# Kernel tuning notes

Measured on AMD Instinct MI355X. Metric: run time of the kernel, lower is better.

Reference implementation:

```python
import jax, jax.numpy as jnp
import numpy as np

N = 100000   # nodes
E = 1000000  # edges
G = 256      # graphs
IN, HID, OUT = 64, 64, 32


def _gcn_conv(x, W, b, src, dst, n_nodes):
    # PyG GCNConv with add_self_loops=True, symmetric normalization:
    # out = D^{-1/2} (A + I) D^{-1/2} X W + b
    h = x @ W  # [N, F]
    deg = jax.ops.segment_sum(jnp.ones_like(src, dtype=h.dtype), dst, num_segments=n_nodes) + 1.0
    dinv = jax.lax.rsqrt(deg)  # deg >= 1 due to self loops
    norm = dinv[src] * dinv[dst]  # [E]
    agg = jax.ops.segment_sum(h[src] * norm[:, None], dst, num_segments=n_nodes)
    agg = agg + h * (dinv * dinv)[:, None]  # self-loop contribution
    return agg + b


def setup_inputs() -> dict:
    key = jax.random.key(0)
    ks = jax.random.split(key, 12)
    x = jax.random.normal(ks[0], (N, IN), dtype=jnp.float32)
    edge_index = jax.random.randint(ks[1], (2, E), 0, N, dtype=jnp.int64)
    batch = jnp.sort(jax.random.randint(ks[2], (N,), 0, G, dtype=jnp.int64))

    def lin(k, fin, fout):
        s = 1.0 / np.sqrt(fin)
        kw, kb = jax.random.split(k)
        return (jax.random.uniform(kw, (fin, fout), minval=-s, maxval=s, dtype=jnp.float32),
                jax.random.uniform(kb, (fout,), minval=-s, maxval=s, dtype=jnp.float32))

    W1, b1 = lin(ks[3], IN, HID)
    W2, b2 = lin(ks[4], HID, HID)
    Wmu, bmu = lin(ks[5], HID, OUT)
    Wlv, blv = lin(ks[6], HID, OUT)
    Wd1, bd1 = lin(ks[7], OUT, HID)
    Wd2, bd2 = lin(ks[8], HID, IN)
    return {"x": x, "edge_index": edge_index, "batch": batch,
            "W1": W1, "b1": b1, "W2": W2, "b2": b2,
            "Wmu": Wmu, "bmu": bmu, "Wlv": Wlv, "blv": blv,
            "Wd1": Wd1, "bd1": bd1, "Wd2": Wd2, "bd2": bd2}


def reference(x, edge_index, batch, W1, b1, W2, b2, Wmu, bmu, Wlv, blv, Wd1, bd1, Wd2, bd2):
    src, dst = edge_index[0], edge_index[1]
    h = jax.nn.relu(_gcn_conv(x, W1, b1, src, dst, N))
    h = jax.nn.relu(_gcn_conv(h, W2, b2, src, dst, N))
    # global mean pool per graph
    sums = jax.ops.segment_sum(h, batch, num_segments=G)
    counts = jax.ops.segment_sum(jnp.ones((N,), dtype=h.dtype), batch, num_segments=G)
    pooled = sums / jnp.maximum(counts, 1.0)[:, None]  # [G, HID]
    mu = pooled @ Wmu + bmu
    logvar = pooled @ Wlv + blv
    eps = jax.random.normal(jax.random.key(42), mu.shape, dtype=mu.dtype)
    z = mu + eps * jnp.exp(0.5 * logvar)
    recon = jax.nn.relu(z @ Wd1 + bd1) @ Wd2 + bd2  # [G, IN]
    return recon, mu, logvar
```

## Files before the change

### kernel.cpp

```cpp
#include <hip/hip_runtime.h>
#include <hip/hip_bf16.h>

typedef __attribute__((ext_vector_type(8))) short bf16x8;
typedef __attribute__((ext_vector_type(4))) float f32x4;

__device__ inline unsigned short f2bf(float f) {
    unsigned u = __float_as_uint(f);
    unsigned r = u + 0x7fffu + ((u >> 16) & 1u);
    return (unsigned short)(r >> 16);
}
__device__ inline float bf2f(unsigned short s) {
    return __uint_as_float((unsigned)s << 16);
}


__device__ inline unsigned rotl32(unsigned x, unsigned r) {
    return (x << r) | (x >> (32 - r));
}

__device__ inline void threefry2x32_042(unsigned c0, unsigned c1,
                                        unsigned& o0, unsigned& o1) {
    const unsigned k0 = 0u, k1 = 42u;
    unsigned ks[3] = { k0, k1, k0 ^ k1 ^ 0x1BD11BDAu };
    unsigned x0 = c0 + ks[0];
    unsigned x1 = c1 + ks[1];
    const unsigned rotA[4] = {13u, 15u, 26u, 6u};
    const unsigned rotB[4] = {17u, 29u, 16u, 24u};

    #pragma unroll
    for (int i = 0; i < 5; ++i) {
        #pragma unroll
        for (int j = 0; j < 4; ++j) {
            unsigned r = (i & 1) ? rotB[j] : rotA[j];
            x0 += x1;
            x1 = rotl32(x1, r);
            x1 ^= x0;
        }
        x0 += ks[(i + 1) % 3];
        x1 += ks[(i + 2) % 3] + (unsigned)(i + 1);
    }
    o0 = x0; o1 = x1;
}

__device__ inline float erfinv_f32(float x) {
    float w = -log1pf(-x * x);
    float p;
    if (w < 5.0f) {
        w -= 2.5f;
        p = 2.81022636e-08f;
        p = fmaf(p, w, 3.43273939e-07f);
        p = fmaf(p, w, -3.5233877e-06f);
        p = fmaf(p, w, -4.39150654e-06f);
        p = fmaf(p, w, 0.00021858087f);
        p = fmaf(p, w, -0.00125372503f);
        p = fmaf(p, w, -0.00417768164f);
        p = fmaf(p, w, 0.246640727f);
        p = fmaf(p, w, 1.50140941f);
    } else {
        w = sqrtf(w) - 3.0f;
        p = -0.000200214257f;
        p = fmaf(p, w, 0.000100950558f);
        p = fmaf(p, w, 0.00134934322f);
        p = fmaf(p, w, -0.00367342844f);
        p = fmaf(p, w, 0.00573950773f);
        p = fmaf(p, w, -0.0076224613f);
        p = fmaf(p, w, 0.00943887047f);
        p = fmaf(p, w, 1.00167406f);
        p = fmaf(p, w, 2.83297682f);
    }
    return p * x;
}

__device__ inline float jax_normal_4232(unsigned idx) {
    unsigned o0, o1;
    threefry2x32_042(0u, idx, o0, o1);
    unsigned bits = o0 ^ o1;
    unsigned fb = (bits >> 9) | 0x3f800000u;
    float f = __uint_as_float(fb) - 1.0f;
    const float lo = -0.99999994f;
    float u = f * (1.0f - lo) + lo;
    u = fmaxf(u, lo);
    return 1.41421356f * erfinv_f32(u);
}


__device__ inline int idx_at(const void* p, long long i, int is64) {
    return is64 ? (int)((const long long*)p)[i] : ((const int*)p)[i];
}

#define NBK 256
#define CAP 4864

__global__ __launch_bounds__(256) void detect_idx64(const unsigned* __restrict__ raw,
                                                    int ne, int* flag,
                                                    int* __restrict__ bcnt,
                                                    int* __restrict__ gcur) {
    __shared__ int nz;
    if (threadIdx.x == 0) nz = 0;
    bcnt[threadIdx.x] = 0;
    gcur[threadIdx.x] = threadIdx.x * CAP;
    __syncthreads();
    int stride = ne / 2048;
    if (stride < 1) stride = 1;
    for (int k = threadIdx.x; k < 2048; k += 256) {
        long long j = (long long)k * stride;
        if (j < ne && raw[2 * j + 1] != 0u) nz = 1;
    }
    __syncthreads();
    if (threadIdx.x == 0) flag[0] = (nz == 0) ? 1 : 0;
}


#define CHUNK_MAX 4096

__global__ __launch_bounds__(256) void bucket_fill(const void* __restrict__ ei,
                                                   const int* __restrict__ flag,
                                                   int* __restrict__ gcur,
                                                   int* __restrict__ bcnt,
                                                   int* __restrict__ pairs,
                                                   int ne, int npb, int chunk) {
    __shared__ int hist[NBK];
    __shared__ int basecur[NBK];
    __shared__ int pbuf[CHUNK_MAX];
    __shared__ unsigned char bbuf[CHUNK_MAX];
    int t = threadIdx.x;
    hist[t] = 0;
    __syncthreads();
    int is64 = flag[0];
    int c0 = blockIdx.x * chunk;
    int c1 = c0 + chunk; if (c1 > ne) c1 = ne;
    for (int i = c0 + t; i < c1; i += 256) {
        int s = idx_at(ei, i, is64);
        int d = idx_at(ei, (long long)ne + i, is64);
        int bb = d / npb;
        int dloc = d - bb * npb;
        pbuf[i - c0] = (dloc << 17) | s;
        bbuf[i - c0] = (unsigned char)bb;
        atomicAdd(&hist[bb], 1);
    }
    __syncthreads();
    if (hist[t] > 0) {
        basecur[t] = atomicAdd(&gcur[t], hist[t]);
        atomicAdd(&bcnt[t], hist[t]);
    }
    __syncthreads();
    int nloc = c1 - c0;
    for (int li = t; li < nloc; li += 256) {
        int bb = bbuf[li];
        int slot = atomicAdd(&basecur[bb], 1);
        if (slot < (bb + 1) * CAP) pairs[slot] = pbuf[li];
    }
}

#define NPB_MAX 512
__global__ __launch_bounds__(256) void csr_build(const int* __restrict__ pairs,
                                                 const int* __restrict__ bcnt,
                                                 int* __restrict__ rowptr,
                                                 int* __restrict__ degarr,
                                                 float* __restrict__ dinv,
                                                 int* __restrict__ csr_src,
                                                 float* __restrict__ sums, int gtot,
                                                 int n, int npb) {
    __shared__ int cnt[NPB_MAX];
    __shared__ int cur[NPB_MAX];
    int b = blockIdx.x;
    int t = threadIdx.x;
    int gi = b * 256 + t;
    if (gi < gtot) sums[gi] = 0.0f;
    int bstart = b * npb;
    int bn = n - bstart; if (bn > npb) bn = npb;
    if (bn <= 0) return;
    int e0 = b * CAP;
    int count = bcnt[b]; if (count > CAP) count = CAP;
    int e1 = e0 + count;

    for (int i = t; i < bn; i += 256) cnt[i] = 0;
    __syncthreads();
    for (int i = e0 + t; i < e1; i += 256)
        atomicAdd(&cnt[pairs[i] >> 17], 1);
    __syncthreads();

    if (t < 64) {
        int running = 0;
        for (int base2 = 0; base2 < bn; base2 += 64) {
            int idx2 = base2 + t;
            int v = (idx2 < bn) ? cnt[idx2] : 0;
            int orig = v;
            #pragma unroll
            for (int off = 1; off < 64; off <<= 1) {
                int tmp = __shfl_up(v, off);
                if (t >= off) v += tmp;
            }
            if (idx2 < bn) cur[idx2] = e0 + running + (v - orig);
            running += __shfl(v, 63);
        }
    }
    __syncthreads();

    for (int ln = t; ln < bn; ln += 256) {
        rowptr[bstart + ln] = cur[ln];
        degarr[bstart + ln] = cnt[ln];
        dinv[bstart + ln] = rsqrtf((float)cnt[ln] + 1.0f);
    }
    __syncthreads();

    for (int i = e0 + t; i < e1; i += 256) {
        int p = pairs[i];
        int slot = atomicAdd(&cur[p >> 17], 1);
        csr_src[slot] = p & 0x1FFFF;
    }
}


__device__ inline void load_wfrags(const float* __restrict__ W,
                                   int cq, int cr, bf16x8 wf[2][4]) {
    #pragma unroll
    for (int ks = 0; ks < 2; ++ks)
        #pragma unroll
        for (int cb = 0; cb < 4; ++cb) {
            bf16x8 v;
            #pragma unroll
            for (int j = 0; j < 8; ++j) {
                int k = ks * 32 + cq * 8 + j;
                v[j] = (short)f2bf(W[k * 64 + cb * 16 + cr]);
            }
            wf[ks][cb] = v;
        }
}

__device__ inline void mfma_store(f32x4 acc[4], const float* __restrict__ dinv,
                                  unsigned short* __restrict__ Y,
                                  int rowbase, int cq, int cr, int nrows) {
    #pragma unroll
    for (int reg = 0; reg < 4; ++reg) {
        int r = rowbase + cq * 4 + reg;
        if (r < nrows) {
            float dv = dinv[r];
            #pragma unroll
            for (int cb = 0; cb < 4; ++cb)
                Y[(size_t)r * 64 + cb * 16 + cr] = f2bf(acc[cb][reg] * dv);
        }
    }
}

__global__ __launch_bounds__(256) void lin64_mfma_f32(const float* __restrict__ X,
                                                      const float* __restrict__ W,
                                                      const float* __restrict__ dinv,
                                                      unsigned short* __restrict__ Y,
                                                      int nrows) {
    int t = threadIdx.x;
    int lane = t & 63, wid = t >> 6;
    int cq = lane >> 4, cr = lane & 15;
    bf16x8 wf[2][4];
    load_wfrags(W, cq, cr, wf);
    int rowbase = (blockIdx.x * 4 + wid) * 16;
    if (rowbase >= nrows) return;
    int arow = rowbase + cr; if (arow >= nrows) arow = nrows - 1;
    const float* xr = X + (size_t)arow * 64;
    bf16x8 af[2];
    #pragma unroll
    for (int ks = 0; ks < 2; ++ks) {
        const float4* p = (const float4*)(xr + ks * 32 + cq * 8);
        float4 a = p[0], b = p[1];
        bf16x8 v;
        v[0] = (short)f2bf(a.x); v[1] = (short)f2bf(a.y);
        v[2] = (short)f2bf(a.z); v[3] = (short)f2bf(a.w);
        v[4] = (short)f2bf(b.x); v[5] = (short)f2bf(b.y);
        v[6] = (short)f2bf(b.z); v[7] = (short)f2bf(b.w);
        af[ks] = v;
    }
    f32x4 z = {0.0f, 0.0f, 0.0f, 0.0f};
    f32x4 acc[4] = {z, z, z, z};
    #pragma unroll
    for (int ks = 0; ks < 2; ++ks)
        #pragma unroll
        for (int cb = 0; cb < 4; ++cb)
            acc[cb] = __builtin_amdgcn_mfma_f32_16x16x32_bf16(af[ks], wf[ks][cb],
                                                              acc[cb], 0, 0, 0);
    mfma_store(acc, dinv, Y, rowbase, cq, cr, nrows);
}

__global__ __launch_bounds__(256) void lin64_mfma_bf16(const unsigned short* __restrict__ X,
                                                       const float* __restrict__ bin,
                                                       const float* __restrict__ W,
                                                       const float* __restrict__ dinv,
                                                       unsigned short* __restrict__ Y,
                                                       int nrows) {
    int t = threadIdx.x;
    int lane = t & 63, wid = t >> 6;
    int cq = lane >> 4, cr = lane & 15;
    bf16x8 wf[2][4];
    load_wfrags(W, cq, cr, wf);
    float bpre[2][8];
    #pragma unroll
    for (int ks = 0; ks < 2; ++ks)
        #pragma unroll
        for (int j = 0; j < 8; ++j)
            bpre[ks][j] = bin[ks * 32 + cq * 8 + j];
    int rowbase = (blockIdx.x * 4 + wid) * 16;
    if (rowbase >= nrows) return;
    int arow = rowbase + cr; if (arow >= nrows) arow = nrows - 1;
    const unsigned short* xr = X + (size_t)arow * 64;
    bf16x8 af[2];
    #pragma unroll
    for (int ks = 0; ks < 2; ++ks) {
        bf16x8 raw = *(const bf16x8*)(xr + ks * 32 + cq * 8);
        bf16x8 v;
        #pragma unroll
        for (int j = 0; j < 8; ++j) {
            float vv = bf2f((unsigned short)raw[j]) + bpre[ks][j];
            v[j] = (short)f2bf(fmaxf(vv, 0.0f));
        }
        af[ks] = v;
    }
    f32x4 z = {0.0f, 0.0f, 0.0f, 0.0f};
    f32x4 acc[4] = {z, z, z, z};
    #pragma unroll
    for (int ks = 0; ks < 2; ++ks)
        #pragma unroll
        for (int cb = 0; cb < 4; ++cb)
            acc[cb] = __builtin_amdgcn_mfma_f32_16x16x32_bf16(af[ks], wf[ks][cb],
                                                              acc[cb], 0, 0, 0);
    mfma_store(acc, dinv, Y, rowbase, cq, cr, nrows);
}


__device__ inline float tree16(const float v[16]) {
    float s0 = (v[0] + v[1]) + (v[2] + v[3]);
    float s1 = (v[4] + v[5]) + (v[6] + v[7]);
    float s2 = (v[8] + v[9]) + (v[10] + v[11]);
    float s3 = (v[12] + v[13]) + (v[14] + v[15]);
    return (s0 + s1) + (s2 + s3);
}

__device__ inline float gather_rounds(const unsigned short* __restrict__ A,
                                      int c, int sl, int f, int start) {
    float acc = 0.0f;
    for (int j0 = start; j0 < f; j0 += 16) {
        int mm = f - j0; if (mm > 16) mm = 16;
        int sidx[16];
        #pragma unroll
        for (int j = 0; j < 16; ++j) sidx[j] = __shfl(sl, j < mm ? j0 + j : 0);
        float v[16];
        #pragma unroll
        for (int j = 0; j < 16; ++j) v[j] = bf2f(A[(size_t)sidx[j] * 64 + c]);
        #pragma unroll
        for (int j = 0; j < 16; ++j) v[j] = (j < mm) ? v[j] : 0.0f;
        acc += tree16(v);
    }
    return acc;
}

__global__ __launch_bounds__(256) void gcn_gather(const unsigned short* __restrict__ A,
                                                  const float* __restrict__ dinv,
                                                  const int* __restrict__ rowptr,
                                                  const int* __restrict__ degarr,
                                                  const int* __restrict__ csr_src,
                                                  unsigned short* __restrict__ B, int n) {
    int t = threadIdx.x;
    int wid = t >> 6;
    int c = t & 63;
    int n0 = (blockIdx.x * 4 + wid) * 2;
    if (n0 >= n) return;
    int has1 = (n0 + 1 < n);
    int n1 = has1 ? n0 + 1 : n0;

    float acc0 = bf2f(A[(size_t)n0 * 64 + c]);
    float acc1 = bf2f(A[(size_t)n1 * 64 + c]);
    int beg0 = rowptr[n0], m0 = degarr[n0];
    int beg1 = rowptr[n1], m1 = has1 ? degarr[n1] : 0;

    int f0 = m0 > 64 ? 64 : m0;
    int f1 = m1 > 64 ? 64 : m1;
    int sl0 = (c < f0) ? csr_src[beg0 + c] : 0;
    int sl1 = (c < f1) ? csr_src[beg1 + c] : 0;

    {
        int mm0 = f0 > 16 ? 16 : f0;
        int mm1 = f1 > 16 ? 16 : f1;
        int s0i[16], s1i[16];
        #pragma unroll
        for (int j = 0; j < 16; ++j) {
            s0i[j] = __shfl(sl0, j < mm0 ? j : 0);
            s1i[j] = __shfl(sl1, j < mm1 ? j : 0);
        }
        float v0[16], v1[16];
        #pragma unroll
        for (int j = 0; j < 16; ++j) v0[j] = bf2f(A[(size_t)s0i[j] * 64 + c]);
        #pragma unroll
        for (int j = 0; j < 16; ++j) v1[j] = bf2f(A[(size_t)s1i[j] * 64 + c]);
        #pragma unroll
        for (int j = 0; j < 16; ++j) {
            v0[j] = (j < mm0) ? v0[j] : 0.0f;
            v1[j] = (j < mm1) ? v1[j] : 0.0f;
        }
        acc0 += tree16(v0);
        acc1 += tree16(v1);
    }

    if (f0 > 16) acc0 += gather_rounds(A, c, sl0, f0, 16);
    for (int chunk = 64; chunk < m0; chunk += 64) {
        int rem = m0 - chunk; int f = rem > 64 ? 64 : rem;
        int sl = (c < f) ? csr_src[beg0 + chunk + c] : 0;
        acc0 += gather_rounds(A, c, sl, f, 0);
    }
    if (f1 > 16) acc1 += gather_rounds(A, c, sl1, f1, 16);
    for (int chunk = 64; chunk < m1; chunk += 64) {
        int rem = m1 - chunk; int f = rem > 64 ? 64 : rem;
        int sl = (c < f) ? csr_src[beg1 + chunk + c] : 0;
        acc1 += gather_rounds(A, c, sl, f, 0);
    }

    B[(size_t)n0 * 64 + c] = f2bf(acc0 * dinv[n0]);
    if (has1) B[(size_t)n1 * 64 + c] = f2bf(acc1 * dinv[n1]);
}

#define POOL_NPW 16
__global__ __launch_bounds__(256) void pool_seg(const __hip_bfloat16* __restrict__ X,
                                                const float* __restrict__ b,
                                                const void* __restrict__ batch,
                                                const int* __restrict__ flag,
                                                float* __restrict__ sums,
                                                float* __restrict__ counts, int n) {
    int t = threadIdx.x;
    int c = t & 63;
    int wid = blockIdx.x * 4 + (t >> 6);
    int s0 = wid * POOL_NPW;
    if (s0 >= n) return;
    int s1 = s0 + POOL_NPW; if (s1 > n) s1 = n;
    int is64 = flag[0];
    float bc = b[c];
    float acc = 0.0f, cnt = 0.0f;
    int cur = idx_at(batch, s0, is64);
    int i = s0;
    for (; i + 4 <= s1; i += 4) {
        int g0 = idx_at(batch, i + 0, is64);
        int g1 = idx_at(batch, i + 1, is64);
        int g2 = idx_at(batch, i + 2, is64);
        int g3 = idx_at(batch, i + 3, is64);
        float v0 = __bfloat162float(X[(size_t)(i + 0) * 64 + c]);
        float v1 = __bfloat162float(X[(size_t)(i + 1) * 64 + c]);
        float v2 = __bfloat162float(X[(size_t)(i + 2) * 64 + c]);
        float v3 = __bfloat162float(X[(size_t)(i + 3) * 64 + c]);
        if (g0 != cur) {
            atomicAdd(&sums[(size_t)cur * 64 + c], acc);
            if (c == 0) atomicAdd(&counts[cur], cnt);
            acc = 0.0f; cnt = 0.0f; cur = g0;
        }
        acc += fmaxf(v0 + bc, 0.0f); cnt += 1.0f;
        if (g1 != cur) {
            atomicAdd(&sums[(size_t)cur * 64 + c], acc);
            if (c == 0) atomicAdd(&counts[cur], cnt);
            acc = 0.0f; cnt = 0.0f; cur = g1;
        }
        acc += fmaxf(v1 + bc, 0.0f); cnt += 1.0f;
        if (g2 != cur) {
            atomicAdd(&sums[(size_t)cur * 64 + c], acc);
            if (c == 0) atomicAdd(&counts[cur], cnt);
            acc = 0.0f; cnt = 0.0f; cur = g2;
        }
        acc += fmaxf(v2 + bc, 0.0f); cnt += 1.0f;
        if (g3 != cur) {
            atomicAdd(&sums[(size_t)cur * 64 + c], acc);
            if (c == 0) atomicAdd(&counts[cur], cnt);
            acc = 0.0f; cnt = 0.0f; cur = g3;
        }
        acc += fmaxf(v3 + bc, 0.0f); cnt += 1.0f;
    }
    for (; i < s1; ++i) {
        int g0 = idx_at(batch, i, is64);
        float v0 = __bfloat162float(X[(size_t)i * 64 + c]);
        if (g0 != cur) {
            atomicAdd(&sums[(size_t)cur * 64 + c], acc);
            if (c == 0) atomicAdd(&counts[cur], cnt);
            acc = 0.0f; cnt = 0.0f; cur = g0;
        }
        acc += fmaxf(v0 + bc, 0.0f); cnt += 1.0f;
    }
    atomicAdd(&sums[(size_t)cur * 64 + c], acc);
    if (c == 0) atomicAdd(&counts[cur], cnt);
}

__global__ __launch_bounds__(64) void vae_head(const float* __restrict__ sums,
                                               const float* __restrict__ counts,
                                               const float* __restrict__ Wmu,
                                               const float* __restrict__ bmu,
                                               const float* __restrict__ Wlv,
                                               const float* __restrict__ blv,
                                               const float* __restrict__ Wd1,
                                               const float* __restrict__ bd1,
                                               const float* __restrict__ Wd2,
                                               const float* __restrict__ bd2,
                                               float* __restrict__ out) {
    int g = blockIdx.x;
    int t = threadIdx.x;
    __shared__ float sp[64];
    __shared__ float sz[32];
    __shared__ float sh[64];

    float cnt = fmaxf(counts[g], 1.0f);
    sp[t] = sums[(size_t)g * 64 + t] / cnt;
    __syncthreads();

    if (t < 32) {
        float mu = bmu[t];
        float lv = blv[t];
        #pragma unroll
        for (int k = 0; k < 64; ++k) {
            float pk = sp[k];
            mu = fmaf(pk, Wmu[k * 32 + t], mu);
            lv = fmaf(pk, Wlv[k * 32 + t], lv);
        }
        unsigned idx = (unsigned)(g * 32 + t);
        float eps = jax_normal_4232(idx);
        float z = fmaf(eps, expf(0.5f * lv), mu);
        sz[t] = z;
        out[16384 + (size_t)g * 32 + t] = mu;
        out[24576 + (size_t)g * 32 + t] = lv;
    }
    __syncthreads();

    float h = bd1[t];
    #pragma unroll
    for (int k = 0; k < 32; ++k) h = fmaf(sz[k], Wd1[k * 64 + t], h);
    h = fmaxf(h, 0.0f);
    sh[t] = h;
    __syncthreads();

    float r = bd2[t];
    #pragma unroll
    for (int k = 0; k < 64; ++k) r = fmaf(sh[k], Wd2[k * 64 + t], r);
    out[(size_t)g * 64 + t] = r;
}


extern "C" void kernel_launch(void* const* d_in, const int* in_sizes, int n_in,
                              void* d_out, int out_size, void* d_ws, size_t ws_size,
                              hipStream_t stream) {
    const float* x    = (const float*)d_in[0];
    const void*  ei   = d_in[1];
    const void*  batch= d_in[2];
    const float* W1   = (const float*)d_in[3];
    const float* b1   = (const float*)d_in[4];
    const float* W2   = (const float*)d_in[5];
    const float* b2   = (const float*)d_in[6];
    const float* Wmu  = (const float*)d_in[7];
    const float* bmu  = (const float*)d_in[8];
    const float* Wlv  = (const float*)d_in[9];
    const float* blv  = (const float*)d_in[10];
    const float* Wd1  = (const float*)d_in[11];
    const float* bd1  = (const float*)d_in[12];
    const float* Wd2  = (const float*)d_in[13];
    const float* bd2  = (const float*)d_in[14];

    const int N = in_sizes[0] / 64;
    const int E = in_sizes[1] / 2;
    const int G = 256;

    const int NPB = (N + NBK - 1) / NBK;
    const int nbu = (N + NPB - 1) / NPB;

    float* out = (float*)d_out;

    float* dinv = (float*)d_ws;
    __hip_bfloat16* A = (__hip_bfloat16*)(dinv + ((N + 255) & ~255));
    __hip_bfloat16* B = A + (size_t)N * 64;
    float* sums = (float*)(B + (size_t)N * 64);
    float* cnts = sums + (size_t)G * 64;
    int*   flag = (int*)(cnts + G);
    int*   rowptr = flag + 256;
    int*   degarr = rowptr + ((N + 255) & ~255);
    int*   bcnt = degarr + ((N + 255) & ~255);
    int*   gcur = bcnt + 256;
    int*   csr_src = gcur + 256;
    int*   pairs = csr_src + (size_t)nbu * CAP;

    const int blkGather = (N + 7) / 8;
    const int blkLin   = (N + 63) / 64;
    const int blkPool  = (N + POOL_NPW * 4 - 1) / (POOL_NPW * 4);
    const int chunkE   = (E + NBK - 1) / NBK;
    const int gtot     = G * 64 + G;

    detect_idx64<<<1, 256, 0, stream>>>((const unsigned*)ei, E, flag, bcnt, gcur);

    bucket_fill<<<NBK, 256, 0, stream>>>(ei, flag, gcur, bcnt, pairs, E, NPB, chunkE);
    csr_build<<<nbu, 256, 0, stream>>>(pairs, bcnt, rowptr, degarr, dinv, csr_src,
                                       sums, gtot, N, NPB);

    lin64_mfma_f32<<<blkLin, 256, 0, stream>>>(x, W1, dinv, (unsigned short*)A, N);
    gcn_gather<<<blkGather, 256, 0, stream>>>((const unsigned short*)A, dinv,
                                              rowptr, degarr, csr_src,
                                              (unsigned short*)B, N);

    lin64_mfma_bf16<<<blkLin, 256, 0, stream>>>((const unsigned short*)B, b1, W2,
                                                dinv, (unsigned short*)A, N);
    gcn_gather<<<blkGather, 256, 0, stream>>>((const unsigned short*)A, dinv,
                                              rowptr, degarr, csr_src,
                                              (unsigned short*)B, N);

    pool_seg<<<blkPool, 256, 0, stream>>>(B, b2, batch, flag, sums, cnts, N);
    vae_head<<<G, 64, 0, stream>>>(sums, cnts, Wmu, bmu, Wlv, blv,
                                   Wd1, bd1, Wd2, bd2, out);
}
```

Measured before the change: 162.2 us.

## Split node features into four 16-column slabs and gather per slab

Node feature buffers now use a slab layout: four column blocks of 16 bf16 values each, every block stored contiguously over all nodes. The gather kernel runs a 2D grid with one slab per blockIdx.y and gives each 16-lane group its own node, so each slab array (N×16 bf16, about 3.2 MB) is small enough to stay cache-resident during the random neighbour gathers. The linear and pooling kernels are updated to read and write the slab layout. In exchange, each gathered row is only 32 bytes wide, the CSR indices are read four times, and wave-level imbalance comes from taking the maximum degree over four nodes.

```diff
diff --git a/kernel.cpp b/kernel.cpp
--- a/kernel.cpp
+++ b/kernel.cpp
@@ -230,7 +230,8 @@
 
 __device__ inline void mfma_store(f32x4 acc[4], const float* __restrict__ dinv,
                                   unsigned short* __restrict__ Y,
-                                  int rowbase, int cq, int cr, int nrows) {
+                                  int rowbase, int cq, int cr, int nrows,
+                                  size_t n16) {
     #pragma unroll
     for (int reg = 0; reg < 4; ++reg) {
         int r = rowbase + cq * 4 + reg;
@@ -238,7 +239,7 @@
             float dv = dinv[r];
             #pragma unroll
             for (int cb = 0; cb < 4; ++cb)
-                Y[(size_t)r * 64 + cb * 16 + cr] = f2bf(acc[cb][reg] * dv);
+                Y[(size_t)cb * n16 + (size_t)r * 16 + cr] = f2bf(acc[cb][reg] * dv);
         }
     }
 }
@@ -251,6 +252,7 @@
     int t = threadIdx.x;
     int lane = t & 63, wid = t >> 6;
     int cq = lane >> 4, cr = lane & 15;
+    size_t n16 = (size_t)nrows * 16;
     bf16x8 wf[2][4];
     load_wfrags(W, cq, cr, wf);
     int rowbase = (blockIdx.x * 4 + wid) * 16;
@@ -277,7 +279,7 @@
         for (int cb = 0; cb < 4; ++cb)
             acc[cb] = __builtin_amdgcn_mfma_f32_16x16x32_bf16(af[ks], wf[ks][cb],
                                                               acc[cb], 0, 0, 0);
-    mfma_store(acc, dinv, Y, rowbase, cq, cr, nrows);
+    mfma_store(acc, dinv, Y, rowbase, cq, cr, nrows, n16);
 }
 
 __global__ __launch_bounds__(256) void lin64_mfma_bf16(const unsigned short* __restrict__ X,
@@ -289,6 +291,7 @@
     int t = threadIdx.x;
     int lane = t & 63, wid = t >> 6;
     int cq = lane >> 4, cr = lane & 15;
+    size_t n16 = (size_t)nrows * 16;
     bf16x8 wf[2][4];
     load_wfrags(W, cq, cr, wf);
     float bpre[2][8];
@@ -300,11 +303,12 @@
     int rowbase = (blockIdx.x * 4 + wid) * 16;
     if (rowbase >= nrows) return;
     int arow = rowbase + cr; if (arow >= nrows) arow = nrows - 1;
-    const unsigned short* xr = X + (size_t)arow * 64;
     bf16x8 af[2];
     #pragma unroll
     for (int ks = 0; ks < 2; ++ks) {
-        bf16x8 raw = *(const bf16x8*)(xr + ks * 32 + cq * 8);
+        int cbk = ks * 2 + (cq >> 1);
+        const bf16x8 raw = *(const bf16x8*)(X + (size_t)cbk * n16 +
+                                            (size_t)arow * 16 + (cq & 1) * 8);
         bf16x8 v;
         #pragma unroll
         for (int j = 0; j < 8; ++j) {
@@ -321,7 +325,7 @@
         for (int cb = 0; cb < 4; ++cb)
             acc[cb] = __builtin_amdgcn_mfma_f32_16x16x32_bf16(af[ks], wf[ks][cb],
                                                               acc[cb], 0, 0, 0);
-    mfma_store(acc, dinv, Y, rowbase, cq, cr, nrows);
+    mfma_store(acc, dinv, Y, rowbase, cq, cr, nrows, n16);
 }
 
 
@@ -333,86 +337,43 @@
     return (s0 + s1) + (s2 + s3);
 }
 
-__device__ inline float gather_rounds(const unsigned short* __restrict__ A,
-                                      int c, int sl, int f, int start) {
-    float acc = 0.0f;
-    for (int j0 = start; j0 < f; j0 += 16) {
-        int mm = f - j0; if (mm > 16) mm = 16;
+__global__ __launch_bounds__(256) void gcn_gather_sl(const unsigned short* __restrict__ A,
+                                                     const float* __restrict__ dinv,
+                                                     const int* __restrict__ rowptr,
+                                                     const int* __restrict__ degarr,
+                                                     const int* __restrict__ csr_src,
+                                                     unsigned short* __restrict__ B, int n) {
+    int t = threadIdx.x;
+    size_t n16 = (size_t)n * 16;
+    const unsigned short* As = A + (size_t)blockIdx.y * n16;
+    unsigned short* Bs = B + (size_t)blockIdx.y * n16;
+    int wid = t >> 6;
+    int sub = (t >> 4) & 3;
+    int cl = t & 15;
+    int node = (blockIdx.x * 4 + wid) * 4 + sub;
+    int vnode = node < n ? node : n - 1;
+    float acc = bf2f(As[(size_t)vnode * 16 + cl]);
+    int beg = rowptr[vnode];
+    int m = (node < n) ? degarr[vnode] : 0;
+    int mA = __shfl(m, 0), mB = __shfl(m, 16);
+    int mC = __shfl(m, 32), mD = __shfl(m, 48);
+    int mw = max(max(mA, mB), max(mC, mD));
+    for (int j0 = 0; j0 < mw; j0 += 16) {
+        int e = j0 + cl;
+        int eidx = beg + (e < m ? e : (m > 0 ? m - 1 : 0));
+        int sl = csr_src[eidx];
+        int mm = m - j0;
         int sidx[16];
         #pragma unroll
-        for (int j = 0; j < 16; ++j) sidx[j] = __shfl(sl, j < mm ? j0 + j : 0);
+        for (int j = 0; j < 16; ++j) sidx[j] = __shfl(sl, j, 16);
         float v[16];
         #pragma unroll
-        for (int j = 0; j < 16; ++j) v[j] = bf2f(A[(size_t)sidx[j] * 64 + c]);
+        for (int j = 0; j < 16; ++j) v[j] = bf2f(As[(size_t)sidx[j] * 16 + cl]);
         #pragma unroll
         for (int j = 0; j < 16; ++j) v[j] = (j < mm) ? v[j] : 0.0f;
         acc += tree16(v);
     }
-    return acc;
-}
-
-__global__ __launch_bounds__(256) void gcn_gather(const unsigned short* __restrict__ A,
-                                                  const float* __restrict__ dinv,
-                                                  const int* __restrict__ rowptr,
-                                                  const int* __restrict__ degarr,
-                                                  const int* __restrict__ csr_src,
-                                                  unsigned short* __restrict__ B, int n) {
-    int t = threadIdx.x;
-    int wid = t >> 6;
-    int c = t & 63;
-    int n0 = (blockIdx.x * 4 + wid) * 2;
-    if (n0 >= n) return;
-    int has1 = (n0 + 1 < n);
-    int n1 = has1 ? n0 + 1 : n0;
-
-    float acc0 = bf2f(A[(size_t)n0 * 64 + c]);
-    float acc1 = bf2f(A[(size_t)n1 * 64 + c]);
-    int beg0 = rowptr[n0], m0 = degarr[n0];
-    int beg1 = rowptr[n1], m1 = has1 ? degarr[n1] : 0;
-
-    int f0 = m0 > 64 ? 64 : m0;
-    int f1 = m1 > 64 ? 64 : m1;
-    int sl0 = (c < f0) ? csr_src[beg0 + c] : 0;
-    int sl1 = (c < f1) ? csr_src[beg1 + c] : 0;
-
-    {
-        int mm0 = f0 > 16 ? 16 : f0;
-        int mm1 = f1 > 16 ? 16 : f1;
-        int s0i[16], s1i[16];
-        #pragma unroll
-        for (int j = 0; j < 16; ++j) {
-            s0i[j] = __shfl(sl0, j < mm0 ? j : 0);
-            s1i[j] = __shfl(sl1, j < mm1 ? j : 0);
-        }
-        float v0[16], v1[16];
-        #pragma unroll
-        for (int j = 0; j < 16; ++j) v0[j] = bf2f(A[(size_t)s0i[j] * 64 + c]);
-        #pragma unroll
-        for (int j = 0; j < 16; ++j) v1[j] = bf2f(A[(size_t)s1i[j] * 64 + c]);
-        #pragma unroll
-        for (int j = 0; j < 16; ++j) {
-            v0[j] = (j < mm0) ? v0[j] : 0.0f;
-            v1[j] = (j < mm1) ? v1[j] : 0.0f;
-        }
-        acc0 += tree16(v0);
-        acc1 += tree16(v1);
-    }
-
-    if (f0 > 16) acc0 += gather_rounds(A, c, sl0, f0, 16);
-    for (int chunk = 64; chunk < m0; chunk += 64) {
-        int rem = m0 - chunk; int f = rem > 64 ? 64 : rem;
-        int sl = (c < f) ? csr_src[beg0 + chunk + c] : 0;
-        acc0 += gather_rounds(A, c, sl, f, 0);
-    }
-    if (f1 > 16) acc1 += gather_rounds(A, c, sl1, f1, 16);
-    for (int chunk = 64; chunk < m1; chunk += 64) {
-        int rem = m1 - chunk; int f = rem > 64 ? 64 : rem;
-        int sl = (c < f) ? csr_src[beg1 + chunk + c] : 0;
-        acc1 += gather_rounds(A, c, sl, f, 0);
-    }
-
-    B[(size_t)n0 * 64 + c] = f2bf(acc0 * dinv[n0]);
-    if (has1) B[(size_t)n1 * 64 + c] = f2bf(acc1 * dinv[n1]);
+    if (node < n) Bs[(size_t)node * 16 + cl] = f2bf(acc * dinv[node]);
 }
 
 #define POOL_NPW 16
@@ -429,6 +390,8 @@
     if (s0 >= n) return;
     int s1 = s0 + POOL_NPW; if (s1 > n) s1 = n;
     int is64 = flag[0];
+    size_t n16 = (size_t)n * 16;
+    const __hip_bfloat16* Xc = X + (size_t)(c >> 4) * n16 + (c & 15);
     float bc = b[c];
     float acc = 0.0f, cnt = 0.0f;
     int cur = idx_at(batch, s0, is64);
@@ -438,10 +401,10 @@
         int g1 = idx_at(batch, i + 1, is64);
         int g2 = idx_at(batch, i + 2, is64);
         int g3 = idx_at(batch, i + 3, is64);
-        float v0 = __bfloat162float(X[(size_t)(i + 0) * 64 + c]);
-        float v1 = __bfloat162float(X[(size_t)(i + 1) * 64 + c]);
-        float v2 = __bfloat162float(X[(size_t)(i + 2) * 64 + c]);
-        float v3 = __bfloat162float(X[(size_t)(i + 3) * 64 + c]);
+        float v0 = __bfloat162float(Xc[(size_t)(i + 0) * 16]);
+        float v1 = __bfloat162float(Xc[(size_t)(i + 1) * 16]);
+        float v2 = __bfloat162float(Xc[(size_t)(i + 2) * 16]);
+        float v3 = __bfloat162float(Xc[(size_t)(i + 3) * 16]);
         if (g0 != cur) {
             atomicAdd(&sums[(size_t)cur * 64 + c], acc);
             if (c == 0) atomicAdd(&counts[cur], cnt);
@@ -469,7 +432,7 @@
     }
     for (; i < s1; ++i) {
         int g0 = idx_at(batch, i, is64);
-        float v0 = __bfloat162float(X[(size_t)i * 64 + c]);
+        float v0 = __bfloat162float(Xc[(size_t)i * 16]);
         if (g0 != cur) {
             atomicAdd(&sums[(size_t)cur * 64 + c], acc);
             if (c == 0) atomicAdd(&counts[cur], cnt);
@@ -575,11 +538,11 @@
     int*   csr_src = gcur + 256;
     int*   pairs = csr_src + (size_t)nbu * CAP;
 
-    const int blkGather = (N + 7) / 8;
     const int blkLin   = (N + 63) / 64;
     const int blkPool  = (N + POOL_NPW * 4 - 1) / (POOL_NPW * 4);
     const int chunkE   = (E + NBK - 1) / NBK;
     const int gtot     = G * 64 + G;
+    dim3 gridG((N + 15) / 16, 4);
 
     detect_idx64<<<1, 256, 0, stream>>>((const unsigned*)ei, E, flag, bcnt, gcur);
 
@@ -588,15 +551,15 @@
                                        sums, gtot, N, NPB);
 
     lin64_mfma_f32<<<blkLin, 256, 0, stream>>>(x, W1, dinv, (unsigned short*)A, N);
-    gcn_gather<<<blkGather, 256, 0, stream>>>((const unsigned short*)A, dinv,
-                                              rowptr, degarr, csr_src,
-                                              (unsigned short*)B, N);
+    gcn_gather_sl<<<gridG, 256, 0, stream>>>((const unsigned short*)A, dinv,
+                                             rowptr, degarr, csr_src,
+                                             (unsigned short*)B, N);
 
     lin64_mfma_bf16<<<blkLin, 256, 0, stream>>>((const unsigned short*)B, b1, W2,
                                                 dinv, (unsigned short*)A, N);
-    gcn_gather<<<blkGather, 256, 0, stream>>>((const unsigned short*)A, dinv,
-                                              rowptr, degarr, csr_src,
-                                              (unsigned short*)B, N);
+    gcn_gather_sl<<<gridG, 256, 0, stream>>>((const unsigned short*)A, dinv,
+                                             rowptr, degarr, csr_src,
+                                             (unsigned short*)B, N);
 
     pool_seg<<<blkPool, 256, 0, stream>>>(B, b2, batch, flag, sums, cnts, N);
     vae_head<<<G, 64, 0, stream>>>(sums, cnts, Wmu, bmu, Wlv, blv,
```

New measurement: 182.8 us. 12.7% more time.
